# Performance work log

Measured on AMD Instinct MI355X. Metric: run time of the kernel, lower is better.

The kernel has to match this reference:

```python
import jax, jax.numpy as jnp
from jax import lax
import numpy as np


def _conv4d(x, w, b, stride, padding):
    # Faithful 4D conv emulation: K temporal slices, each its own 3D conv.
    # x: [B,Ci,T,D,H,W]; w: [K,Co,Ci,k,k,k]; b: [K,Co] or None.
    # Quirk preserved: bias b[i] is added once per contributing temporal tap i
    # (the torch code accumulates full conv3d outputs including bias).
    B, Ci, T = x.shape[0], x.shape[1], x.shape[2]
    K = w.shape[0]
    O = (T + 2 * padding - K) // stride + 1
    out = None
    for i in range(K):
        j = np.arange(O) * stride + i - padding          # static input frame idx per output frame
        valid = (j >= 0) & (j < T)
        jc = np.clip(j, 0, T - 1)
        xg = jnp.moveaxis(x[:, :, jc], 2, 1)             # [B,O,Ci,D,H,W]
        xg = xg.reshape(B * O, Ci, x.shape[3], x.shape[4], x.shape[5])
        y = lax.conv_general_dilated(xg, w[i], (stride,) * 3, [(padding, padding)] * 3,
                                     dimension_numbers=('NCDHW', 'OIDHW', 'NCDHW'))
        if b is not None:
            y = y + b[i][None, :, None, None, None]
        y = y.reshape(B, O, y.shape[1], y.shape[2], y.shape[3], y.shape[4])
        y = y * jnp.asarray(valid, y.dtype)[None, :, None, None, None, None]
        out = y if out is None else out + y
    return jnp.moveaxis(out, 1, 2)                       # [B,Co,O,D',H',W']


def _maxpool4d(x, k, s, p):
    # pool3d-per-frame then pool1d over T == one 4D max pool (max commutes)
    return lax.reduce_window(x, jnp.array(-jnp.inf, x.dtype), lax.max,
                             (1, 1, k, k, k, k), (1, 1, s, s, s, s),
                             [(0, 0), (0, 0)] + [(p, p)] * 4)


def _avgpool4d_2(x):
    # avg-of-avgs over a full (2,2,2,2) window == 4D average
    s = lax.reduce_window(x, jnp.array(0.0, x.dtype), lax.add,
                          (1, 1, 2, 2, 2, 2), (1,) * 6, [(0, 0)] * 6)
    return s / jnp.asarray(16.0, x.dtype)


def _block(x, w1, b1, w2, b2, stride, dw):
    y = jax.nn.relu(_conv4d(x, w1, b1, stride, 1))
    y = _conv4d(y, w2, b2, 1, 1)
    res = x if dw is None else _conv4d(x, dw, None, stride, 0)
    return jax.nn.relu(y + res)


def _forward(x, conv1_w, l1_w1, l1_b1, l1_w2, l1_b2,
             l2_w1, l2_b1, l2_w2, l2_b2, l2_dw,
             l3_w1, l3_b1, l3_w2, l3_b2, l3_dw,
             l4_w1, l4_b1, l4_w2, l4_b2, l4_dw, fc_w, fc_b):
    h = x[:, None]                                       # [B,1,T,D,H,W]
    h = jax.nn.relu(_conv4d(h, conv1_w, None, 2, 3))     # 36 -> 18
    h = _maxpool4d(h, 3, 2, 1)                           # 18 -> 9
    h = _block(h, l1_w1, l1_b1, l1_w2, l1_b2, 1, None)   # 9
    h = _block(h, l2_w1, l2_b1, l2_w2, l2_b2, 2, l2_dw)  # 9 -> 5
    h = _block(h, l3_w1, l3_b1, l3_w2, l3_b2, 2, l3_dw)  # 5 -> 3
    h = _block(h, l4_w1, l4_b1, l4_w2, l4_b2, 2, l4_dw)  # 3 -> 2
    h = _avgpool4d_2(h)                                  # 2 -> 1
    h = h.reshape(-1, 512)
    return h @ fc_w.T + fc_b


def setup_inputs() -> dict:
    key = jax.random.key(0)
    ks = jax.random.split(key, 40)
    ctr = iter(range(40))
    def w(shape, fan):
        return jax.random.normal(ks[next(ctr)], shape, jnp.float32) * np.float32(np.sqrt(2.0 / fan))
    def bias(shape):
        return jax.random.normal(ks[next(ctr)], shape, jnp.float32) * np.float32(0.01)
    d = {}
    d['x'] = jax.random.normal(ks[next(ctr)], (1, 36, 36, 36, 36), jnp.float32)
    d['conv1_w'] = w((7, 64, 1, 7, 7, 7), 343)
    d['l1_w1'] = w((3, 64, 64, 3, 3, 3), 64 * 27); d['l1_b1'] = bias((3, 64))
    d['l1_w2'] = w((3, 64, 64, 3, 3, 3), 64 * 27); d['l1_b2'] = bias((3, 64))
    d['l2_w1'] = w((3, 128, 64, 3, 3, 3), 64 * 27); d['l2_b1'] = bias((3, 128))
    d['l2_w2'] = w((3, 128, 128, 3, 3, 3), 128 * 27); d['l2_b2'] = bias((3, 128))
    d['l2_dw'] = w((1, 128, 64, 1, 1, 1), 64)
    d['l3_w1'] = w((3, 256, 128, 3, 3, 3), 128 * 27); d['l3_b1'] = bias((3, 256))
    d['l3_w2'] = w((3, 256, 256, 3, 3, 3), 256 * 27); d['l3_b2'] = bias((3, 256))
    d['l3_dw'] = w((1, 256, 128, 1, 1, 1), 128)
    d['l4_w1'] = w((3, 512, 256, 3, 3, 3), 256 * 27); d['l4_b1'] = bias((3, 512))
    d['l4_w2'] = w((3, 512, 512, 3, 3, 3), 512 * 27); d['l4_b2'] = bias((3, 512))
    d['l4_dw'] = w((1, 512, 256, 1, 1, 1), 256)
    d['fc_w'] = w((1, 512), 512); d['fc_b'] = bias((1,))
    return d


def reference(x, conv1_w, l1_w1, l1_b1, l1_w2, l1_b2,
              l2_w1, l2_b1, l2_w2, l2_b2, l2_dw,
              l3_w1, l3_b1, l3_w2, l3_b2, l3_dw,
              l4_w1, l4_b1, l4_w2, l4_b2, l4_dw, fc_w, fc_b):
    return _forward(x, conv1_w, l1_w1, l1_b1, l1_w2, l1_b2,
                    l2_w1, l2_b1, l2_w2, l2_b2, l2_dw,
                    l3_w1, l3_b1, l3_w2, l3_b2, l3_dw,
                    l4_w1, l4_b1, l4_w2, l4_b2, l4_dw, fc_w, fc_b)
```

## Files before the change

kernel.cpp:

```cpp
#include <hip/hip_runtime.h>

typedef __bf16 bf16x8 __attribute__((ext_vector_type(8)));
typedef float f32x4 __attribute__((ext_vector_type(4)));
typedef unsigned short ushortT;

__device__ __forceinline__ unsigned short f2bf(float f) {
    unsigned u = __float_as_uint(f);
    u += 0x7fffu + ((u >> 16) & 1u);
    return (unsigned short)(u >> 16);
}
__device__ __forceinline__ float bf2f(unsigned short h) {
    return __uint_as_float((unsigned)h << 16);
}

__global__ __launch_bounds__(256) void prep0(const float* __restrict__ x,
                                             const float* __restrict__ c1w,
                                             ushortT* __restrict__ xp,
                                             ushortT* __restrict__ o1) {
    int bid = blockIdx.x, tid = threadIdx.x;
    if (bid < 1737) {
        long idx = (long)bid * 256 + tid;
        if (idx >= 444528L) return;
        int q = (int)(idx % 6); long r = idx / 6;
        int h = (int)(r % 42); r /= 42;
        int d = (int)(r % 42); int t = (int)(r / 42);
        int tt = t - 3, dd = d - 3, hh = h - 3;
        bool rok = ((unsigned)tt < 36u) && ((unsigned)dd < 36u) && ((unsigned)hh < 36u);
        const float* src = x + (((long)tt * 36 + dd) * 36 + hh) * 36;
        union { ushortT s[8]; uint4 u; } v;
#pragma unroll
        for (int j = 0; j < 8; ++j) {
            int ww = q * 8 + j - 3;
            float f = (rok && (unsigned)ww < 36u) ? src[ww] : 0.f;
            v.s[j] = f2bf(f);
        }
        *(uint4*)(xp + idx * 8) = v.u;
    } else {
        int e = (bid - 1737) * 256 + tid;
        if (e < 200704) {
            int k = e % 3136, co = e / 3136;
            int kw = k & 7, kh = (k >> 3) & 7, kdt = k >> 6;
            int kt = kdt / 7, kd = kdt % 7;
            float v = 0.f;
            if (kh < 7 && kw < 7)
                v = c1w[(size_t)(kt * 64 + co) * 343 + kd * 49 + kh * 7 + kw];
            o1[e] = f2bf(v);
        }
    }
}

__global__ __launch_bounds__(128) void mega_kernel(
        const ushortT* __restrict__ xp, const ushortT* __restrict__ aw,
        ushortT* __restrict__ outc1,
        const float* __restrict__ w11, const float* __restrict__ w12,
        const float* __restrict__ w21, const float* __restrict__ w22,
        const float* __restrict__ w31, const float* __restrict__ w32,
        const float* __restrict__ w41, const float* __restrict__ w42,
        ushortT* __restrict__ o11, ushortT* __restrict__ o12,
        ushortT* __restrict__ o21, ushortT* __restrict__ o22,
        ushortT* __restrict__ o31, ushortT* __restrict__ o32,
        ushortT* __restrict__ o41, ushortT* __restrict__ o42) {
    __shared__ __align__(16) ushortT smem[10472];
    int bid = blockIdx.x, tid = threadIdx.x;

    if (bid < 1350) {
        int wt = bid % 5; int r = bid / 5;
        int ht = r % 5; r /= 5;
        int dt = r % 3; int ot = r / 3;
        int ow0 = wt * 4, oh0 = ht * 4, od0 = dt * 6;
        int gw0 = 2 * ow0, gh0 = 2 * oh0, gd0 = 2 * od0;

        int lane = tid & 63, wv = tid >> 6;
        int l15 = lane & 15, g = lane >> 4;
        int dh = l15 >> 2, dw = l15 & 3;

        const ushortT* ap0 = aw + (size_t)(wv * 32 + l15) * 3136 + g * 8;
        const ushortT* ap1 = ap0 + 16 * 3136;

        ushortT* curb = smem;
        ushortT* nxtb = smem + 5236;

        auto stage = [&](ushortT* buf, int kt) {
            int gt = 2 * ot + kt;
            for (int rr = tid; rr < 238; rr += 128) {
                int ld = rr / 14, lh = rr - ld * 14;
                const ushortT* s = xp +
                    ((size_t)((gt * 42 + gd0 + ld) * 42 + gh0 + lh)) * 48 + gw0;
                uint4 a = *(const uint4*)s;
                uint4 b = *(const uint4*)(s + 8);
                unsigned* d = (unsigned*)buf + rr * 11;
                d[0] = a.x; d[1] = a.y; d[2] = a.z; d[3] = a.w;
                d[4] = b.x; d[5] = b.y; d[6] = b.z; d[7] = b.w;
            }
        };

        f32x4 acc[2][6];
#pragma unroll
        for (int c = 0; c < 2; ++c)
#pragma unroll
            for (int m = 0; m < 6; ++m) acc[c][m] = (f32x4){0.f, 0.f, 0.f, 0.f};

        stage(curb, 0);
        __syncthreads();

        int lhl = (2 * dh + g) * 22 + 2 * dw;
        int kidx = 0;
        for (int kt = 0; kt < 7; ++kt) {
            if (kt < 6) stage(nxtb, kt + 1);
            for (int kd = 0; kd < 7; ++kd) {
                int C0 = kd * 308 + lhl;
#pragma unroll
                for (int khq = 0; khq < 2; ++khq) {
                    bf16x8 a0 = *(const bf16x8*)(ap0 + kidx);
                    bf16x8 a1 = *(const bf16x8*)(ap1 + kidx);
                    kidx += 32;
                    int C = C0 + khq * 88;
#pragma unroll
                    for (int m = 0; m < 6; ++m) {
                        int off = C + m * 616;
                        union { unsigned u[4]; bf16x8 v; } bb;
                        bb.u[0] = *(const unsigned*)(curb + off);
                        bb.u[1] = *(const unsigned*)(curb + off + 2);
                        bb.u[2] = *(const unsigned*)(curb + off + 4);
                        bb.u[3] = *(const unsigned*)(curb + off + 6);
                        acc[0][m] = __builtin_amdgcn_mfma_f32_16x16x32_bf16(a0, bb.v, acc[0][m], 0, 0, 0);
                        acc[1][m] = __builtin_amdgcn_mfma_f32_16x16x32_bf16(a1, bb.v, acc[1][m], 0, 0, 0);
                    }
                }
            }
            __syncthreads();
            ushortT* t2 = curb; curb = nxtb; nxtb = t2;
        }

        int oh = oh0 + dh, ow = ow0 + dw;
        if (oh < 18 && ow < 18) {
#pragma unroll
            for (int m = 0; m < 6; ++m) {
                int od = od0 + m;
                int pos = ((ot * 18 + od) * 18 + oh) * 18 + ow;
#pragma unroll
                for (int c = 0; c < 2; ++c) {
                    ushort4 st;
                    st.x = f2bf(fmaxf(acc[c][m][0], 0.f));
                    st.y = f2bf(fmaxf(acc[c][m][1], 0.f));
                    st.z = f2bf(fmaxf(acc[c][m][2], 0.f));
                    st.w = f2bf(fmaxf(acc[c][m][3], 0.f));
                    *(ushort4*)(outc1 + (size_t)pos * 64 + wv * 32 + c * 16 + g * 4) = st;
                }
            }
        }
        return;
    }

    int wb = bid - 1350;
    const float* in; ushortT* out; int Ci, Co, nc, base;
    if (wb < 1536) {
        if (wb < 384) {
            if (wb < 192) { in = w11; out = o11; Ci = 64; Co = 64; nc = 1; base = 0; }
            else          { in = w12; out = o12; Ci = 64; Co = 64; nc = 1; base = 192; }
        } else if (wb < 768) { in = w21; out = o21; Ci = 64;  Co = 128; nc = 1; base = 384; }
        else                 { in = w22; out = o22; Ci = 128; Co = 128; nc = 2; base = 768; }
    } else if (wb < 6144) {
        if (wb < 3072) { in = w31; out = o31; Ci = 128; Co = 256; nc = 2; base = 1536; }
        else           { in = w32; out = o32; Ci = 256; Co = 256; nc = 4; base = 3072; }
    } else {
        if (wb < 12288) { in = w41; out = o41; Ci = 256; Co = 512; nc = 4; base = 6144; }
        else            { in = w42; out = o42; Ci = 512; Co = 512; nc = 8; base = 12288; }
    }
    int lb = wb - base;
    int c64 = lb % nc;
    int co = (lb / nc) % Co;
    int i = lb / (nc * Co);

    const float* src = in + ((size_t)(i * Co + co) * Ci + 64 * c64) * 27;
    float* tile = (float*)smem;
    for (int e = tid; e < 432; e += 128)
        *(float4*)(tile + 4 * e) = *(const float4*)(src + 4 * e);
    __syncthreads();
    ushortT* dst = out + (size_t)(i * 27) * Co * Ci + (size_t)co * Ci + 64 * c64;
    size_t tapstride = (size_t)Co * Ci;
    for (int e = tid; e < 432; e += 128) {
        int tap = e >> 4, q = e & 15;
        ushort4 v;
        v.x = f2bf(tile[(4 * q + 0) * 27 + tap]);
        v.y = f2bf(tile[(4 * q + 1) * 27 + tap]);
        v.z = f2bf(tile[(4 * q + 2) * 27 + tap]);
        v.w = f2bf(tile[(4 * q + 3) * 27 + tap]);
        *(ushort4*)(dst + (size_t)tap * tapstride + 4 * q) = v;
    }
}

__global__ void maxpool2(const ushortT* __restrict__ in, ushortT* __restrict__ out,
                         ushortT* __restrict__ zb) {
    int idx = blockIdx.x * 256 + threadIdx.x;
    if (idx < 128) zb[idx] = 0;
    if (idx >= 6561 * 16) return;
    int c4 = idx & 15;
    int p = idx >> 4;
    int ow = p % 9; int t = p / 9;
    int oh = t % 9; t /= 9;
    int od = t % 9; int ot = t / 9;
    ushort4 m = {0, 0, 0, 0};
    for (int kt = 0; kt < 3; ++kt) { int it = 2 * ot + kt - 1; if ((unsigned)it >= 18u) continue;
        for (int kd = 0; kd < 3; ++kd) { int id = 2 * od + kd - 1; if ((unsigned)id >= 18u) continue;
            for (int kh = 0; kh < 3; ++kh) { int ih = 2 * oh + kh - 1; if ((unsigned)ih >= 18u) continue;
                int rb = ((it * 18 + id) * 18 + ih) * 18;
                for (int kw = 0; kw < 3; ++kw) { int iw = 2 * ow + kw - 1; if ((unsigned)iw >= 18u) continue;
                    ushort4 v = *(const ushort4*)(in + (size_t)(rb + iw) * 64 + c4 * 4);
                    m.x = v.x > m.x ? v.x : m.x;
                    m.y = v.y > m.y ? v.y : m.y;
                    m.z = v.z > m.z ? v.z : m.z;
                    m.w = v.w > m.w ? v.w : m.w;
                }
            }
        }
    }
    *(ushort4*)(out + (size_t)p * 64 + c4 * 4) = m;
}

template <int KC, int FUSE>
__global__ void convmfma(const ushortT* __restrict__ xb, const ushortT* __restrict__ wt,
                         const float* __restrict__ bias, const ushortT* __restrict__ res,
                         ushortT* __restrict__ outb, float* __restrict__ part,
                         const ushortT* __restrict__ zq,
                         int Ci, int Co, int T, int O, int stride, int chunk,
                         const float* __restrict__ dwW, ushortT* __restrict__ dwOut) {
    if (dwW && blockIdx.y == (unsigned)(Co >> 6)) {
        int O2 = O * O, O3 = O2 * O, O4 = O3 * O;
        int total = Co * O4;
        int sthr = gridDim.x * gridDim.z * 256;
        for (int idx = (blockIdx.z * gridDim.x + blockIdx.x) * 256 + threadIdx.x;
             idx < total; idx += sthr) {
            int co = idx % Co;
            int pos = idx / Co;
            int ow = pos % O, oh = (pos / O) % O, od = (pos / O2) % O, ot = pos / O3;
            int ip = (((2 * ot) * T + 2 * od) * T + 2 * oh) * T + 2 * ow;
            const ushortT* xpp = xb + (size_t)ip * Ci;
            const float* wp = dwW + (size_t)co * Ci;
            float acc = 0.f;
            for (int c8 = 0; c8 < Ci; c8 += 8) {
                uint4 xv = *(const uint4*)(xpp + c8);
                float4 w0 = *(const float4*)(wp + c8);
                float4 w1 = *(const float4*)(wp + c8 + 4);
                acc = fmaf(bf2f((unsigned short)(xv.x & 0xffff)), w0.x, acc);
                acc = fmaf(bf2f((unsigned short)(xv.x >> 16)),    w0.y, acc);
                acc = fmaf(bf2f((unsigned short)(xv.y & 0xffff)), w0.z, acc);
                acc = fmaf(bf2f((unsigned short)(xv.y >> 16)),    w0.w, acc);
                acc = fmaf(bf2f((unsigned short)(xv.z & 0xffff)), w1.x, acc);
                acc = fmaf(bf2f((unsigned short)(xv.z >> 16)),    w1.y, acc);
                acc = fmaf(bf2f((unsigned short)(xv.w & 0xffff)), w1.z, acc);
                acc = fmaf(bf2f((unsigned short)(xv.w >> 16)),    w1.w, acc);
            }
            dwOut[idx] = f2bf(acc);
        }
        return;
    }

    int lane = threadIdx.x & 63;
    int wv = threadIdx.x >> 6;
    int p0 = blockIdx.x * 16;
    int co0 = (blockIdx.y * 4 + wv) * 16;
    int cbase = blockIdx.z * chunk;

    int pn = p0 + (lane & 15);
    int O2 = O * O, O3 = O2 * O, O4 = O3 * O;
    bool pv = pn < O4;
    int pc = pv ? pn : 0;
    int ow = pc % O, oh = (pc / O) % O, od = (pc / O2) % O, ot = pc / O3;
    int g = lane >> 4;
    int kl = cbase + g * 8;

    const ushortT* aRow = wt + (size_t)(co0 + (lane & 15)) * Ci + kl;
    size_t tapStride = (size_t)Co * Ci;
    const ushortT* zp = zq + g * 8;

    f32x4 acc[4];
#pragma unroll
    for (int a = 0; a < 4; ++a) acc[a] = (f32x4){0.f, 0.f, 0.f, 0.f};

    int itb = ot * stride - 1, idb = od * stride - 1, ihb = oh * stride - 1, iwb = ow * stride - 1;

#pragma unroll
    for (int i = 0; i < 3; ++i) {
        int it = itb + i;
        bool vt = pv && ((unsigned)it < (unsigned)T);
#pragma unroll
        for (int kd = 0; kd < 3; ++kd) {
            int id = idb + kd;
            bool vdd = vt && ((unsigned)id < (unsigned)T);
            int btd = (it * T + id) * T;
#pragma unroll
            for (int kh = 0; kh < 3; ++kh) {
                int ih = ihb + kh;
                bool vh = vdd && ((unsigned)ih < (unsigned)T);
#pragma unroll
                for (int kw = 0; kw < 3; ++kw) {
                    int iw = iwb + kw;
                    bool v = vh && ((unsigned)iw < (unsigned)T);
                    int ip = (btd + ih) * T + iw;
                    const ushortT* bp = v ? (xb + (size_t)ip * Ci + kl) : zp;
                    const int tap = (i * 9 + kd * 3 + kh) * 3 + kw;
                    const ushortT* apw = aRow + (size_t)tap * tapStride;
#pragma unroll
                    for (int kc = 0; kc < KC; ++kc) {
                        bf16x8 av = *(const bf16x8*)(apw + kc * 32);
                        bf16x8 bv = *(const bf16x8*)(bp + kc * 32);
                        acc[(tap * KC + kc) & 3] =
                            __builtin_amdgcn_mfma_f32_16x16x32_bf16(av, bv, acc[(tap * KC + kc) & 3], 0, 0, 0);
                    }
                }
            }
        }
    }

    if (!pv) return;
    f32x4 asum = acc[0];
#pragma unroll
    for (int a = 1; a < 4; ++a) {
        asum[0] += acc[a][0]; asum[1] += acc[a][1];
        asum[2] += acc[a][2]; asum[3] += acc[a][3];
    }
    int cob = co0 + g * 4;
    if (FUSE) {
        float bb[4] = {0.f, 0.f, 0.f, 0.f};
        for (int i = 0; i < 3; ++i) {
            int it = itb + i;
            if ((unsigned)it < (unsigned)T) {
#pragma unroll
                for (int rr = 0; rr < 4; ++rr) bb[rr] += bias[i * Co + cob + rr];
            }
        }
        float rv[4] = {0.f, 0.f, 0.f, 0.f};
        if (res) {
            ushort4 r4 = *(const ushort4*)(res + (size_t)pn * Co + cob);
            rv[0] = bf2f(r4.x); rv[1] = bf2f(r4.y); rv[2] = bf2f(r4.z); rv[3] = bf2f(r4.w);
        }
        ushort4 st;
        st.x = f2bf(fmaxf(asum[0] + bb[0] + rv[0], 0.f));
        st.y = f2bf(fmaxf(asum[1] + bb[1] + rv[1], 0.f));
        st.z = f2bf(fmaxf(asum[2] + bb[2] + rv[2], 0.f));
        st.w = f2bf(fmaxf(asum[3] + bb[3] + rv[3], 0.f));
        *(ushort4*)(outb + (size_t)pn * Co + cob) = st;
    } else {
        *(f32x4*)(part + ((size_t)blockIdx.z * O4 + pn) * Co + cob) = asum;
    }
}

__global__ void finalize_k(const float* __restrict__ part, int KS,
                           const float* __restrict__ bias, const ushortT* __restrict__ res,
                           ushortT* __restrict__ outb, int Co, int O4, int T, int O, int stride,
                           int total) {
    int idx = blockIdx.x * 256 + threadIdx.x;
    if (idx >= total) return;
    int co = idx % Co;
    int pos = idx / Co;
    float v = 0.f;
    for (int z = 0; z < KS; ++z) v += part[((size_t)z * O4 + pos) * Co + co];
    int ot = pos / (O * O * O);
    for (int i = 0; i < 3; ++i) {
        int it = ot * stride + i - 1;
        if ((unsigned)it < (unsigned)T) v += bias[i * Co + co];
    }
    if (res) v += bf2f(res[idx]);
    outb[idx] = f2bf(fmaxf(v, 0.f));
}

__global__ void avgfc2(const ushortT* __restrict__ xin, const float* __restrict__ fw,
                       const float* __restrict__ fb, float* __restrict__ out) {
    __shared__ float ls[8];
    int t = threadIdx.x;
    float s = 0.f;
#pragma unroll
    for (int pp = 0; pp < 16; ++pp) s += bf2f(xin[pp * 512 + t]);
    s = s * (1.f / 16.f) * fw[t];
    for (int off = 32; off > 0; off >>= 1) s += __shfl_xor(s, off, 64);
    if ((t & 63) == 0) ls[t >> 6] = s;
    __syncthreads();
    if (t == 0) {
        float tot = 0.f;
#pragma unroll
        for (int i = 0; i < 8; ++i) tot += ls[i];
        out[0] = tot + fb[0];
    }
}

extern "C" void kernel_launch(void* const* d_in, const int* in_sizes, int n_in,
                              void* d_out, int out_size, void* d_ws, size_t ws_size,
                              hipStream_t stream) {
    const float* x       = (const float*)d_in[0];
    const float* conv1_w = (const float*)d_in[1];
    const float* l1_w1 = (const float*)d_in[2];
    const float* l1_b1 = (const float*)d_in[3];
    const float* l1_w2 = (const float*)d_in[4];
    const float* l1_b2 = (const float*)d_in[5];
    const float* l2_w1 = (const float*)d_in[6];
    const float* l2_b1 = (const float*)d_in[7];
    const float* l2_w2 = (const float*)d_in[8];
    const float* l2_b2 = (const float*)d_in[9];
    const float* l2_dw = (const float*)d_in[10];
    const float* l3_w1 = (const float*)d_in[11];
    const float* l3_b1 = (const float*)d_in[12];
    const float* l3_w2 = (const float*)d_in[13];
    const float* l3_b2 = (const float*)d_in[14];
    const float* l3_dw = (const float*)d_in[15];
    const float* l4_w1 = (const float*)d_in[16];
    const float* l4_b1 = (const float*)d_in[17];
    const float* l4_w2 = (const float*)d_in[18];
    const float* l4_b2 = (const float*)d_in[19];
    const float* l4_dw = (const float*)d_in[20];
    const float* fc_w  = (const float*)d_in[21];
    const float* fc_b  = (const float*)d_in[22];
    float* outp = (float*)d_out;

    char* bp = (char*)d_ws;
    auto alloc = [&](size_t bytes) {
        char* r = bp;
        bp += (bytes + 255) & ~(size_t)255;
        return (void*)r;
    };
    ushortT* A16 = (ushortT*)alloc(6718464ull * 2);
    ushortT* XP  = (ushortT*)alloc(3556224ull * 2);
    ushortT* Aw1 = (ushortT*)alloc(200704ull * 2);
    ushortT* X0 = (ushortT*)alloc(419904ull * 2);
    ushortT* Y1 = (ushortT*)alloc(419904ull * 2);
    ushortT* X1 = (ushortT*)alloc(419904ull * 2);
    ushortT* Y2 = (ushortT*)alloc(80000ull * 2);
    ushortT* R2 = (ushortT*)alloc(80000ull * 2);
    ushortT* X2 = (ushortT*)alloc(80000ull * 2);
    ushortT* Y3 = (ushortT*)alloc(20736ull * 2);
    ushortT* R3 = (ushortT*)alloc(20736ull * 2);
    ushortT* X3 = (ushortT*)alloc(20736ull * 2);
    ushortT* Y4 = (ushortT*)alloc(8192ull * 2);
    ushortT* R4 = (ushortT*)alloc(8192ull * 2);
    ushortT* X4 = (ushortT*)alloc(8192ull * 2);
    ushortT* W11 = (ushortT*)alloc(331776ull * 2);
    ushortT* W12 = (ushortT*)alloc(331776ull * 2);
    ushortT* W21 = (ushortT*)alloc(663552ull * 2);
    ushortT* W22 = (ushortT*)alloc(1327104ull * 2);
    ushortT* W31 = (ushortT*)alloc(2654208ull * 2);
    ushortT* W32 = (ushortT*)alloc(5308416ull * 2);
    ushortT* W41 = (ushortT*)alloc(10616832ull * 2);
    ushortT* W42 = (ushortT*)alloc(21233664ull * 2);
    float* P    = (float*)alloc(165888ull * 4);
    ushortT* ZB = (ushortT*)alloc(256);
    if ((size_t)(bp - (char*)d_ws) > ws_size) return;

    prep0<<<2521, 256, 0, stream>>>(x, conv1_w, XP, Aw1);

    mega_kernel<<<25926, 128, 0, stream>>>(XP, Aw1, A16,
                                           l1_w1, l1_w2, l2_w1, l2_w2, l3_w1, l3_w2,
                                           l4_w1, l4_w2,
                                           W11, W12, W21, W22, W31, W32, W41, W42);

    maxpool2<<<411, 256, 0, stream>>>(A16, X0, ZB);

    convmfma<2, 1><<<dim3(411, 1, 1), 256, 0, stream>>>(X0, W11, l1_b1, nullptr, Y1, nullptr,
                                                        ZB, 64, 64, 9, 9, 1, 64,
                                                        nullptr, nullptr);
    convmfma<2, 1><<<dim3(411, 1, 1), 256, 0, stream>>>(Y1, W12, l1_b2, X0, X1, nullptr,
                                                        ZB, 64, 64, 9, 9, 1, 64,
                                                        nullptr, nullptr);

    convmfma<2, 1><<<dim3(40, 3, 1), 256, 0, stream>>>(X1, W21, l2_b1, nullptr, Y2, nullptr,
                                                       ZB, 64, 128, 9, 5, 2, 64,
                                                       l2_dw, R2);
    convmfma<4, 1><<<dim3(40, 2, 1), 256, 0, stream>>>(Y2, W22, l2_b2, R2, X2, nullptr,
                                                       ZB, 128, 128, 5, 5, 1, 128,
                                                       nullptr, nullptr);

    convmfma<1, 0><<<dim3(6, 5, 4), 256, 0, stream>>>(X2, W31, nullptr, nullptr, nullptr, P,
                                                      ZB, 128, 256, 5, 3, 2, 32,
                                                      l3_dw, R3);
    finalize_k<<<81, 256, 0, stream>>>(P, 4, l3_b1, nullptr, Y3, 256, 81, 5, 3, 2, 20736);
    convmfma<1, 0><<<dim3(6, 4, 8), 256, 0, stream>>>(Y3, W32, nullptr, nullptr, nullptr, P,
                                                      ZB, 256, 256, 3, 3, 1, 32,
                                                      nullptr, nullptr);
    finalize_k<<<81, 256, 0, stream>>>(P, 8, l3_b2, R3, X3, 256, 81, 3, 3, 1, 20736);

    convmfma<1, 0><<<dim3(1, 9, 8), 256, 0, stream>>>(X3, W41, nullptr, nullptr, nullptr, P,
                                                      ZB, 256, 512, 3, 2, 2, 32,
                                                      l4_dw, R4);
    finalize_k<<<32, 256, 0, stream>>>(P, 8, l4_b1, nullptr, Y4, 512, 16, 3, 2, 2, 8192);
    convmfma<1, 0><<<dim3(1, 8, 16), 256, 0, stream>>>(Y4, W42, nullptr, nullptr, nullptr, P,
                                                       ZB, 512, 512, 2, 2, 1, 32,
                                                       nullptr, nullptr);
    finalize_k<<<32, 256, 0, stream>>>(P, 16, l4_b2, R4, X4, 512, 16, 2, 2, 1, 8192);

    avgfc2<<<1, 512, 0, stream>>>(X4, fc_w, fc_b, outp);
}
```

Before: 558.3 us.

## Fuse split-K finalize into consumer convs and precompute per-frame bias sums

The separate finalize kernels for layers 3 and 4 are removed. Each consumer conv (and the final avg+fc kernel) now reduces the split-K partials, adds the precomputed temporal bias sum and residual, and applies ReLU while loading its input operand. Per-output-frame bias sums are computed once in prep0. The mega_kernel shared-memory row pitch also shrinks from 11 to 9 words, cutting LDS footprint. This saves four launches and intermediate bf16 round trips, but the partial sums are recomputed redundantly for every tap that reads them.

```diff
diff --git a/kernel.cpp b/kernel.cpp
--- a/kernel.cpp
+++ b/kernel.cpp
@@ -15,8 +15,16 @@
 
 __global__ __launch_bounds__(256) void prep0(const float* __restrict__ x,
                                              const float* __restrict__ c1w,
+                                             const float* __restrict__ b31,
+                                             const float* __restrict__ b32,
+                                             const float* __restrict__ b41,
+                                             const float* __restrict__ b42,
                                              ushortT* __restrict__ xp,
-                                             ushortT* __restrict__ o1) {
+                                             ushortT* __restrict__ o1,
+                                             float* __restrict__ BS3a,
+                                             float* __restrict__ BS3b,
+                                             float* __restrict__ BS4a,
+                                             float* __restrict__ BS4b) {
     int bid = blockIdx.x, tid = threadIdx.x;
     if (bid < 1737) {
         long idx = (long)bid * 256 + tid;
@@ -35,7 +43,7 @@
             v.s[j] = f2bf(f);
         }
         *(uint4*)(xp + idx * 8) = v.u;
-    } else {
+    } else if (bid < 2521) {
         int e = (bid - 1737) * 256 + tid;
         if (e < 200704) {
             int k = e % 3136, co = e / 3136;
@@ -45,6 +53,29 @@
             if (kh < 7 && kw < 7)
                 v = c1w[(size_t)(kt * 64 + co) * 343 + kd * 49 + kh * 7 + kw];
             o1[e] = f2bf(v);
+        }
+    } else {
+        int e = (bid - 2521) * 256 + tid;
+        if (e >= 3584) return;
+        auto bsum = [&](const float* b, int Co, int ot, int co, int stride, int Tsrc) {
+            float s = 0.f;
+            for (int i = 0; i < 3; ++i) {
+                int it = ot * stride + i - 1;
+                if ((unsigned)it < (unsigned)Tsrc) s += b[i * Co + co];
+            }
+            return s;
+        };
+        if (e < 768) {
+            BS3a[e] = bsum(b31, 256, e / 256, e % 256, 2, 5);
+        } else if (e < 1536) {
+            int e2 = e - 768;
+            BS3b[e2] = bsum(b32, 256, e2 / 256, e2 % 256, 1, 3);
+        } else if (e < 2560) {
+            int e2 = e - 1536;
+            BS4a[e2] = bsum(b41, 512, e2 / 512, e2 % 512, 2, 3);
+        } else {
+            int e2 = e - 2560;
+            BS4b[e2] = bsum(b42, 512, e2 / 512, e2 % 512, 1, 2);
         }
     }
 }
@@ -60,7 +91,7 @@
         ushortT* __restrict__ o21, ushortT* __restrict__ o22,
         ushortT* __restrict__ o31, ushortT* __restrict__ o32,
         ushortT* __restrict__ o41, ushortT* __restrict__ o42) {
-    __shared__ __align__(16) ushortT smem[10472];
+    __shared__ __align__(16) ushortT smem[8568];
     int bid = blockIdx.x, tid = threadIdx.x;
 
     if (bid < 1350) {
@@ -78,7 +109,7 @@
         const ushortT* ap1 = ap0 + 16 * 3136;
 
         ushortT* curb = smem;
-        ushortT* nxtb = smem + 5236;
+        ushortT* nxtb = smem + 4284;
 
         auto stage = [&](ushortT* buf, int kt) {
             int gt = 2 * ot + kt;
@@ -88,7 +119,7 @@
                     ((size_t)((gt * 42 + gd0 + ld) * 42 + gh0 + lh)) * 48 + gw0;
                 uint4 a = *(const uint4*)s;
                 uint4 b = *(const uint4*)(s + 8);
-                unsigned* d = (unsigned*)buf + rr * 11;
+                unsigned* d = (unsigned*)buf + rr * 9;
                 d[0] = a.x; d[1] = a.y; d[2] = a.z; d[3] = a.w;
                 d[4] = b.x; d[5] = b.y; d[6] = b.z; d[7] = b.w;
             }
@@ -103,21 +134,21 @@
         stage(curb, 0);
         __syncthreads();
 
-        int lhl = (2 * dh + g) * 22 + 2 * dw;
+        int lhl = (2 * dh + g) * 18 + 2 * dw;
         int kidx = 0;
         for (int kt = 0; kt < 7; ++kt) {
             if (kt < 6) stage(nxtb, kt + 1);
             for (int kd = 0; kd < 7; ++kd) {
-                int C0 = kd * 308 + lhl;
+                int C0 = kd * 252 + lhl;
 #pragma unroll
                 for (int khq = 0; khq < 2; ++khq) {
                     bf16x8 a0 = *(const bf16x8*)(ap0 + kidx);
                     bf16x8 a1 = *(const bf16x8*)(ap1 + kidx);
                     kidx += 32;
-                    int C = C0 + khq * 88;
+                    int C = C0 + khq * 72;
 #pragma unroll
                     for (int m = 0; m < 6; ++m) {
-                        int off = C + m * 616;
+                        int off = C + m * 504;
                         union { unsigned u[4]; bf16x8 v; } bb;
                         bb.u[0] = *(const unsigned*)(curb + off);
                         bb.u[1] = *(const unsigned*)(curb + off + 2);
@@ -218,13 +249,40 @@
     *(ushort4*)(out + (size_t)p * 64 + c4 * 4) = m;
 }
 
-template <int KC, int FUSE>
+template <int KS>
+__device__ __forceinline__ void fin8f(const float* __restrict__ Pin, int O4p, int Ci,
+                                      int ip, int kl, const float* __restrict__ BS,
+                                      int ot, const ushortT* __restrict__ resf,
+                                      float* s) {
+    const float* bs = BS + ot * Ci + kl;
+#pragma unroll
+    for (int j = 0; j < 8; ++j) s[j] = bs[j];
+    if (resf) {
+#pragma unroll
+        for (int j = 0; j < 8; ++j) s[j] += bf2f(resf[(size_t)ip * Ci + kl + j]);
+    }
+#pragma unroll
+    for (int z = 0; z < KS; ++z) {
+        const float* p = Pin + ((size_t)z * O4p + ip) * Ci + kl;
+        float4 a = *(const float4*)p;
+        float4 b = *(const float4*)(p + 4);
+        s[0] += a.x; s[1] += a.y; s[2] += a.z; s[3] += a.w;
+        s[4] += b.x; s[5] += b.y; s[6] += b.z; s[7] += b.w;
+    }
+#pragma unroll
+    for (int j = 0; j < 8; ++j) s[j] = fmaxf(s[j], 0.f);
+}
+
+template <int KC, int FUSE, int FINKS>
 __global__ void convmfma(const ushortT* __restrict__ xb, const ushortT* __restrict__ wt,
                          const float* __restrict__ bias, const ushortT* __restrict__ res,
                          ushortT* __restrict__ outb, float* __restrict__ part,
                          const ushortT* __restrict__ zq,
                          int Ci, int Co, int T, int O, int stride, int chunk,
-                         const float* __restrict__ dwW, ushortT* __restrict__ dwOut) {
+                         const float* __restrict__ dwW, ushortT* __restrict__ dwOut,
+                         const float* __restrict__ Pin, const float* __restrict__ BS,
+                         const ushortT* __restrict__ resf) {
+    int T2 = T * T, T3 = T2 * T, T4 = T3 * T;
     if (dwW && blockIdx.y == (unsigned)(Co >> 6)) {
         int O2 = O * O, O3 = O2 * O, O4 = O3 * O;
         int total = Co * O4;
@@ -235,21 +293,31 @@
             int pos = idx / Co;
             int ow = pos % O, oh = (pos / O) % O, od = (pos / O2) % O, ot = pos / O3;
             int ip = (((2 * ot) * T + 2 * od) * T + 2 * oh) * T + 2 * ow;
-            const ushortT* xpp = xb + (size_t)ip * Ci;
             const float* wp = dwW + (size_t)co * Ci;
             float acc = 0.f;
-            for (int c8 = 0; c8 < Ci; c8 += 8) {
-                uint4 xv = *(const uint4*)(xpp + c8);
-                float4 w0 = *(const float4*)(wp + c8);
-                float4 w1 = *(const float4*)(wp + c8 + 4);
-                acc = fmaf(bf2f((unsigned short)(xv.x & 0xffff)), w0.x, acc);
-                acc = fmaf(bf2f((unsigned short)(xv.x >> 16)),    w0.y, acc);
-                acc = fmaf(bf2f((unsigned short)(xv.y & 0xffff)), w0.z, acc);
-                acc = fmaf(bf2f((unsigned short)(xv.y >> 16)),    w0.w, acc);
-                acc = fmaf(bf2f((unsigned short)(xv.z & 0xffff)), w1.x, acc);
-                acc = fmaf(bf2f((unsigned short)(xv.z >> 16)),    w1.y, acc);
-                acc = fmaf(bf2f((unsigned short)(xv.w & 0xffff)), w1.z, acc);
-                acc = fmaf(bf2f((unsigned short)(xv.w >> 16)),    w1.w, acc);
+            if constexpr (FINKS == 0) {
+                const ushortT* xpp = xb + (size_t)ip * Ci;
+                for (int c8 = 0; c8 < Ci; c8 += 8) {
+                    uint4 xv = *(const uint4*)(xpp + c8);
+                    float4 w0 = *(const float4*)(wp + c8);
+                    float4 w1 = *(const float4*)(wp + c8 + 4);
+                    acc = fmaf(bf2f((unsigned short)(xv.x & 0xffff)), w0.x, acc);
+                    acc = fmaf(bf2f((unsigned short)(xv.x >> 16)),    w0.y, acc);
+                    acc = fmaf(bf2f((unsigned short)(xv.y & 0xffff)), w0.z, acc);
+                    acc = fmaf(bf2f((unsigned short)(xv.y >> 16)),    w0.w, acc);
+                    acc = fmaf(bf2f((unsigned short)(xv.z & 0xffff)), w1.x, acc);
+                    acc = fmaf(bf2f((unsigned short)(xv.z >> 16)),    w1.y, acc);
+                    acc = fmaf(bf2f((unsigned short)(xv.w & 0xffff)), w1.z, acc);
+                    acc = fmaf(bf2f((unsigned short)(xv.w >> 16)),    w1.w, acc);
+                }
+            } else {
+                int ots = ip / T3;
+                for (int c8 = 0; c8 < Ci; c8 += 8) {
+                    float s[8];
+                    fin8f<FINKS>(Pin, T4, Ci, ip, c8, BS, ots, resf, s);
+#pragma unroll
+                    for (int j = 0; j < 8; ++j) acc = fmaf(s[j], wp[c8 + j], acc);
+                }
             }
             dwOut[idx] = f2bf(acc);
         }
@@ -298,13 +366,25 @@
                     int iw = iwb + kw;
                     bool v = vh && ((unsigned)iw < (unsigned)T);
                     int ip = (btd + ih) * T + iw;
-                    const ushortT* bp = v ? (xb + (size_t)ip * Ci + kl) : zp;
                     const int tap = (i * 9 + kd * 3 + kh) * 3 + kw;
                     const ushortT* apw = aRow + (size_t)tap * tapStride;
 #pragma unroll
                     for (int kc = 0; kc < KC; ++kc) {
                         bf16x8 av = *(const bf16x8*)(apw + kc * 32);
-                        bf16x8 bv = *(const bf16x8*)(bp + kc * 32);
+                        bf16x8 bv;
+                        if constexpr (FINKS == 0) {
+                            const ushortT* bp = v ? (xb + (size_t)ip * Ci + kl) : zp;
+                            bv = *(const bf16x8*)(bp + kc * 32);
+                        } else {
+                            int ipc = v ? ip : 0;
+                            float s[8];
+                            fin8f<FINKS>(Pin, T4, Ci, ipc, kl + kc * 32, BS, ipc / T3, resf, s);
+                            union { ushortT u[8]; bf16x8 v8; } rb;
+#pragma unroll
+                            for (int j = 0; j < 8; ++j)
+                                rb.u[j] = v ? f2bf(s[j]) : (ushortT)0;
+                            bv = rb.v8;
+                        }
                         acc[(tap * KC + kc) & 3] =
                             __builtin_amdgcn_mfma_f32_16x16x32_bf16(av, bv, acc[(tap * KC + kc) & 3], 0, 0, 0);
                     }
@@ -314,12 +394,10 @@
     }
 
     if (!pv) return;
-    f32x4 asum = acc[0];
-#pragma unroll
-    for (int a = 1; a < 4; ++a) {
-        asum[0] += acc[a][0]; asum[1] += acc[a][1];
-        asum[2] += acc[a][2]; asum[3] += acc[a][3];
-    }
+    f32x4 asum;
+#pragma unroll
+    for (int r = 0; r < 4; ++r)
+        asum[r] = (acc[0][r] + acc[1][r]) + (acc[2][r] + acc[3][r]);
     int cob = co0 + g * 4;
     if (FUSE) {
         float bb[4] = {0.f, 0.f, 0.f, 0.f};
@@ -346,32 +424,18 @@
     }
 }
 
-__global__ void finalize_k(const float* __restrict__ part, int KS,
-                           const float* __restrict__ bias, const ushortT* __restrict__ res,
-                           ushortT* __restrict__ outb, int Co, int O4, int T, int O, int stride,
-                           int total) {
-    int idx = blockIdx.x * 256 + threadIdx.x;
-    if (idx >= total) return;
-    int co = idx % Co;
-    int pos = idx / Co;
-    float v = 0.f;
-    for (int z = 0; z < KS; ++z) v += part[((size_t)z * O4 + pos) * Co + co];
-    int ot = pos / (O * O * O);
-    for (int i = 0; i < 3; ++i) {
-        int it = ot * stride + i - 1;
-        if ((unsigned)it < (unsigned)T) v += bias[i * Co + co];
-    }
-    if (res) v += bf2f(res[idx]);
-    outb[idx] = f2bf(fmaxf(v, 0.f));
-}
-
-__global__ void avgfc2(const ushortT* __restrict__ xin, const float* __restrict__ fw,
-                       const float* __restrict__ fb, float* __restrict__ out) {
+__global__ void avgfc3(const float* __restrict__ Pin, const float* __restrict__ BS,
+                       const ushortT* __restrict__ R4,
+                       const float* __restrict__ fw, const float* __restrict__ fb,
+                       float* __restrict__ out) {
     __shared__ float ls[8];
     int t = threadIdx.x;
     float s = 0.f;
-#pragma unroll
-    for (int pp = 0; pp < 16; ++pp) s += bf2f(xin[pp * 512 + t]);
+    for (int pp = 0; pp < 16; ++pp) {
+        float v = BS[(pp >> 3) * 512 + t] + bf2f(R4[pp * 512 + t]);
+        for (int z = 0; z < 16; ++z) v += Pin[((size_t)z * 16 + pp) * 512 + t];
+        s += fmaxf(v, 0.f);
+    }
     s = s * (1.f / 16.f) * fw[t];
     for (int off = 32; off > 0; off >>= 1) s += __shfl_xor(s, off, 64);
     if ((t & 63) == 0) ls[t >> 6] = s;
@@ -427,12 +491,8 @@
     ushortT* Y2 = (ushortT*)alloc(80000ull * 2);
     ushortT* R2 = (ushortT*)alloc(80000ull * 2);
     ushortT* X2 = (ushortT*)alloc(80000ull * 2);
-    ushortT* Y3 = (ushortT*)alloc(20736ull * 2);
     ushortT* R3 = (ushortT*)alloc(20736ull * 2);
-    ushortT* X3 = (ushortT*)alloc(20736ull * 2);
-    ushortT* Y4 = (ushortT*)alloc(8192ull * 2);
     ushortT* R4 = (ushortT*)alloc(8192ull * 2);
-    ushortT* X4 = (ushortT*)alloc(8192ull * 2);
     ushortT* W11 = (ushortT*)alloc(331776ull * 2);
     ushortT* W12 = (ushortT*)alloc(331776ull * 2);
     ushortT* W21 = (ushortT*)alloc(663552ull * 2);
@@ -441,11 +501,17 @@
     ushortT* W32 = (ushortT*)alloc(5308416ull * 2);
     ushortT* W41 = (ushortT*)alloc(10616832ull * 2);
     ushortT* W42 = (ushortT*)alloc(21233664ull * 2);
-    float* P    = (float*)alloc(165888ull * 4);
+    float* PA   = (float*)alloc(82944ull * 4);
+    float* PB   = (float*)alloc(165888ull * 4);
+    float* BS3a = (float*)alloc(768ull * 4);
+    float* BS3b = (float*)alloc(768ull * 4);
+    float* BS4a = (float*)alloc(1024ull * 4);
+    float* BS4b = (float*)alloc(1024ull * 4);
     ushortT* ZB = (ushortT*)alloc(256);
     if ((size_t)(bp - (char*)d_ws) > ws_size) return;
 
-    prep0<<<2521, 256, 0, stream>>>(x, conv1_w, XP, Aw1);
+    prep0<<<2535, 256, 0, stream>>>(x, conv1_w, l3_b1, l3_b2, l4_b1, l4_b2,
+                                    XP, Aw1, BS3a, BS3b, BS4a, BS4b);
 
     mega_kernel<<<25926, 128, 0, stream>>>(XP, Aw1, A16,
                                            l1_w1, l1_w2, l2_w1, l2_w2, l3_w1, l3_w2,
@@ -454,37 +520,33 @@
 
     maxpool2<<<411, 256, 0, stream>>>(A16, X0, ZB);
 
-    convmfma<2, 1><<<dim3(411, 1, 1), 256, 0, stream>>>(X0, W11, l1_b1, nullptr, Y1, nullptr,
-                                                        ZB, 64, 64, 9, 9, 1, 64,
-                                                        nullptr, nullptr);
-    convmfma<2, 1><<<dim3(411, 1, 1), 256, 0, stream>>>(Y1, W12, l1_b2, X0, X1, nullptr,
-                                                        ZB, 64, 64, 9, 9, 1, 64,
-                                                        nullptr, nullptr);
-
-    convmfma<2, 1><<<dim3(40, 3, 1), 256, 0, stream>>>(X1, W21, l2_b1, nullptr, Y2, nullptr,
-                                                       ZB, 64, 128, 9, 5, 2, 64,
-                                                       l2_dw, R2);
-    convmfma<4, 1><<<dim3(40, 2, 1), 256, 0, stream>>>(Y2, W22, l2_b2, R2, X2, nullptr,
-                                                       ZB, 128, 128, 5, 5, 1, 128,
-                                                       nullptr, nullptr);
-
-    convmfma<1, 0><<<dim3(6, 5, 4), 256, 0, stream>>>(X2, W31, nullptr, nullptr, nullptr, P,
-                                                      ZB, 128, 256, 5, 3, 2, 32,
-                                                      l3_dw, R3);
-    finalize_k<<<81, 256, 0, stream>>>(P, 4, l3_b1, nullptr, Y3, 256, 81, 5, 3, 2, 20736);
-    convmfma<1, 0><<<dim3(6, 4, 8), 256, 0, stream>>>(Y3, W32, nullptr, nullptr, nullptr, P,
-                                                      ZB, 256, 256, 3, 3, 1, 32,
-                                                      nullptr, nullptr);
-    finalize_k<<<81, 256, 0, stream>>>(P, 8, l3_b2, R3, X3, 256, 81, 3, 3, 1, 20736);
-
-    convmfma<1, 0><<<dim3(1, 9, 8), 256, 0, stream>>>(X3, W41, nullptr, nullptr, nullptr, P,
-                                                      ZB, 256, 512, 3, 2, 2, 32,
-                                                      l4_dw, R4);
-    finalize_k<<<32, 256, 0, stream>>>(P, 8, l4_b1, nullptr, Y4, 512, 16, 3, 2, 2, 8192);
-    convmfma<1, 0><<<dim3(1, 8, 16), 256, 0, stream>>>(Y4, W42, nullptr, nullptr, nullptr, P,
-                                                       ZB, 512, 512, 2, 2, 1, 32,
-                                                       nullptr, nullptr);
-    finalize_k<<<32, 256, 0, stream>>>(P, 16, l4_b2, R4, X4, 512, 16, 2, 2, 1, 8192);
-
-    avgfc2<<<1, 512, 0, stream>>>(X4, fc_w, fc_b, outp);
-}
+    convmfma<2, 1, 0><<<dim3(411, 1, 1), 256, 0, stream>>>(
+        X0, W11, l1_b1, nullptr, Y1, nullptr, ZB, 64, 64, 9, 9, 1, 64,
+        nullptr, nullptr, nullptr, nullptr, nullptr);
+    convmfma<2, 1, 0><<<dim3(411, 1, 1), 256, 0, stream>>>(
+        Y1, W12, l1_b2, X0, X1, nullptr, ZB, 64, 64, 9, 9, 1, 64,
+        nullptr, nullptr, nullptr, nullptr, nullptr);
+
+    convmfma<2, 1, 0><<<dim3(40, 3, 1), 256, 0, stream>>>(
+        X1, W21, l2_b1, nullptr, Y2, nullptr, ZB, 64, 128, 9, 5, 2, 64,
+        l2_dw, R2, nullptr, nullptr, nullptr);
+    convmfma<4, 1, 0><<<dim3(40, 2, 1), 256, 0, stream>>>(
+        Y2, W22, l2_b2, R2, X2, nullptr, ZB, 128, 128, 5, 5, 1, 128,
+        nullptr, nullptr, nullptr, nullptr, nullptr);
+
+    convmfma<1, 0, 0><<<dim3(6, 5, 4), 256, 0, stream>>>(
+        X2, W31, nullptr, nullptr, nullptr, PA, ZB, 128, 256, 5, 3, 2, 32,
+        l3_dw, R3, nullptr, nullptr, nullptr);
+    convmfma<1, 0, 4><<<dim3(6, 4, 8), 256, 0, stream>>>(
+        nullptr, W32, nullptr, nullptr, nullptr, PB, ZB, 256, 256, 3, 3, 1, 32,
+        nullptr, nullptr, PA, BS3a, nullptr);
+
+    convmfma<1, 0, 8><<<dim3(1, 9, 8), 256, 0, stream>>>(
+        nullptr, W41, nullptr, nullptr, nullptr, PA, ZB, 256, 512, 3, 2, 2, 32,
+        l4_dw, R4, PB, BS3b, R3);
+    convmfma<1, 0, 8><<<dim3(1, 8, 16), 256, 0, stream>>>(
+        nullptr, W42, nullptr, nullptr, nullptr, PB, ZB, 512, 512, 2, 2, 1, 32,
+        nullptr, nullptr, PA, BS4a, nullptr);
+
+    avgfc3<<<1, 512, 0, stream>>>(PB, BS4b, R4, fc_w, fc_b, outp);
+}
```

Measured after the change: 798.8 us. 1.43x slower.

## Pre-tile weights into MFMA fragment layout and split layer3/4 convs over taps

Applied to the files above, without the earlier changes.

The weight conversion now writes bf16 weights already arranged as 16x32 MFMA A-fragments, so each lane loads a contiguous 16-byte chunk instead of strided rows. Layer 3 and 4 convolutions are additionally split across 9 (time, depth) tap groups through a new TS template parameter, which multiplies grid size and the number of partial sums the finalize kernel reduces. The stem kernel's LDS row padding drops from 11 to 9 words, reducing shared memory per block. The trade-offs are a much larger partial buffer and more finalize reduction traffic, plus a possible change in LDS bank conflicts.

```diff
diff --git a/kernel.cpp b/kernel.cpp
--- a/kernel.cpp
+++ b/kernel.cpp
@@ -60,7 +60,7 @@
         ushortT* __restrict__ o21, ushortT* __restrict__ o22,
         ushortT* __restrict__ o31, ushortT* __restrict__ o32,
         ushortT* __restrict__ o41, ushortT* __restrict__ o42) {
-    __shared__ __align__(16) ushortT smem[10472];
+    __shared__ __align__(16) ushortT smem[8568];
     int bid = blockIdx.x, tid = threadIdx.x;
 
     if (bid < 1350) {
@@ -78,7 +78,7 @@
         const ushortT* ap1 = ap0 + 16 * 3136;
 
         ushortT* curb = smem;
-        ushortT* nxtb = smem + 5236;
+        ushortT* nxtb = smem + 4284;
 
         auto stage = [&](ushortT* buf, int kt) {
             int gt = 2 * ot + kt;
@@ -88,7 +88,7 @@
                     ((size_t)((gt * 42 + gd0 + ld) * 42 + gh0 + lh)) * 48 + gw0;
                 uint4 a = *(const uint4*)s;
                 uint4 b = *(const uint4*)(s + 8);
-                unsigned* d = (unsigned*)buf + rr * 11;
+                unsigned* d = (unsigned*)buf + rr * 9;
                 d[0] = a.x; d[1] = a.y; d[2] = a.z; d[3] = a.w;
                 d[4] = b.x; d[5] = b.y; d[6] = b.z; d[7] = b.w;
             }
@@ -103,21 +103,21 @@
         stage(curb, 0);
         __syncthreads();
 
-        int lhl = (2 * dh + g) * 22 + 2 * dw;
+        int lhl = (2 * dh + g) * 18 + 2 * dw;
         int kidx = 0;
         for (int kt = 0; kt < 7; ++kt) {
             if (kt < 6) stage(nxtb, kt + 1);
             for (int kd = 0; kd < 7; ++kd) {
-                int C0 = kd * 308 + lhl;
+                int C0 = kd * 252 + lhl;
 #pragma unroll
                 for (int khq = 0; khq < 2; ++khq) {
                     bf16x8 a0 = *(const bf16x8*)(ap0 + kidx);
                     bf16x8 a1 = *(const bf16x8*)(ap1 + kidx);
                     kidx += 32;
-                    int C = C0 + khq * 88;
+                    int C = C0 + khq * 72;
 #pragma unroll
                     for (int m = 0; m < 6; ++m) {
-                        int off = C + m * 616;
+                        int off = C + m * 504;
                         union { unsigned u[4]; bf16x8 v; } bb;
                         bb.u[0] = *(const unsigned*)(curb + off);
                         bb.u[1] = *(const unsigned*)(curb + off + 2);
@@ -177,16 +177,19 @@
     for (int e = tid; e < 432; e += 128)
         *(float4*)(tile + 4 * e) = *(const float4*)(src + 4 * e);
     __syncthreads();
-    ushortT* dst = out + (size_t)(i * 27) * Co * Ci + (size_t)co * Ci + 64 * c64;
-    size_t tapstride = (size_t)Co * Ci;
-    for (int e = tid; e < 432; e += 128) {
-        int tap = e >> 4, q = e & 15;
-        ushort4 v;
-        v.x = f2bf(tile[(4 * q + 0) * 27 + tap]);
-        v.y = f2bf(tile[(4 * q + 1) * 27 + tap]);
-        v.z = f2bf(tile[(4 * q + 2) * 27 + tap]);
-        v.w = f2bf(tile[(4 * q + 3) * 27 + tap]);
-        *(ushort4*)(dst + (size_t)tap * tapstride + 4 * q) = v;
+
+    size_t nCb = Co >> 4, nKb = Ci >> 5;
+    int cb = co >> 4, l15 = co & 15;
+    for (int e = tid; e < 216; e += 128) {
+        int tap = e >> 3, q8 = e & 7;
+        int kb = 2 * c64 + (q8 >> 2);
+        int g = q8 & 3;
+        int tapP = i * 27 + tap;
+        union { ushortT s[8]; uint4 u; } v;
+#pragma unroll
+        for (int j = 0; j < 8; ++j)
+            v.s[j] = f2bf(tile[(q8 * 8 + j) * 27 + tap]);
+        *(uint4*)(out + (((size_t)tapP * nCb + cb) * nKb + kb) * 512 + (g * 16 + l15) * 8) = v.u;
     }
 }
 
@@ -218,7 +221,7 @@
     *(ushort4*)(out + (size_t)p * 64 + c4 * 4) = m;
 }
 
-template <int KC, int FUSE>
+template <int KC, int FUSE, int TS>
 __global__ void convmfma(const ushortT* __restrict__ xb, const ushortT* __restrict__ wt,
                          const float* __restrict__ bias, const ushortT* __restrict__ res,
                          ushortT* __restrict__ outb, float* __restrict__ part,
@@ -259,8 +262,14 @@
     int lane = threadIdx.x & 63;
     int wv = threadIdx.x >> 6;
     int p0 = blockIdx.x * 16;
-    int co0 = (blockIdx.y * 4 + wv) * 16;
-    int cbase = blockIdx.z * chunk;
+    int cb = blockIdx.y * 4 + wv;
+    int co0 = cb * 16;
+    int zz = blockIdx.z;
+    int ks, ts;
+    if (TS > 1) { ks = zz / TS; ts = zz % TS; } else { ks = zz; ts = 0; }
+    int cbase = ks * chunk;
+    int kb0 = cbase >> 5;
+    size_t nCb = Co >> 4, nKb = Ci >> 5;
 
     int pn = p0 + (lane & 15);
     int O2 = O * O, O3 = O2 * O, O4 = O3 * O;
@@ -270,8 +279,6 @@
     int g = lane >> 4;
     int kl = cbase + g * 8;
 
-    const ushortT* aRow = wt + (size_t)(co0 + (lane & 15)) * Ci + kl;
-    size_t tapStride = (size_t)Co * Ci;
     const ushortT* zp = zq + g * 8;
 
     f32x4 acc[4];
@@ -280,46 +287,78 @@
 
     int itb = ot * stride - 1, idb = od * stride - 1, ihb = oh * stride - 1, iwb = ow * stride - 1;
 
-#pragma unroll
-    for (int i = 0; i < 3; ++i) {
-        int it = itb + i;
-        bool vt = pv && ((unsigned)it < (unsigned)T);
-#pragma unroll
-        for (int kd = 0; kd < 3; ++kd) {
-            int id = idb + kd;
-            bool vdd = vt && ((unsigned)id < (unsigned)T);
-            int btd = (it * T + id) * T;
-#pragma unroll
-            for (int kh = 0; kh < 3; ++kh) {
-                int ih = ihb + kh;
-                bool vh = vdd && ((unsigned)ih < (unsigned)T);
-#pragma unroll
-                for (int kw = 0; kw < 3; ++kw) {
-                    int iw = iwb + kw;
-                    bool v = vh && ((unsigned)iw < (unsigned)T);
-                    int ip = (btd + ih) * T + iw;
-                    const ushortT* bp = v ? (xb + (size_t)ip * Ci + kl) : zp;
-                    const int tap = (i * 9 + kd * 3 + kh) * 3 + kw;
-                    const ushortT* apw = aRow + (size_t)tap * tapStride;
-#pragma unroll
-                    for (int kc = 0; kc < KC; ++kc) {
-                        bf16x8 av = *(const bf16x8*)(apw + kc * 32);
-                        bf16x8 bv = *(const bf16x8*)(bp + kc * 32);
-                        acc[(tap * KC + kc) & 3] =
-                            __builtin_amdgcn_mfma_f32_16x16x32_bf16(av, bv, acc[(tap * KC + kc) & 3], 0, 0, 0);
+    if (TS == 1) {
+#pragma unroll
+        for (int i = 0; i < 3; ++i) {
+            int it = itb + i;
+            bool vt = pv && ((unsigned)it < (unsigned)T);
+#pragma unroll
+            for (int kd = 0; kd < 3; ++kd) {
+                int id = idb + kd;
+                bool vdd = vt && ((unsigned)id < (unsigned)T);
+                int btd = (it * T + id) * T;
+#pragma unroll
+                for (int kh = 0; kh < 3; ++kh) {
+                    int ih = ihb + kh;
+                    bool vh = vdd && ((unsigned)ih < (unsigned)T);
+#pragma unroll
+                    for (int kw = 0; kw < 3; ++kw) {
+                        int iw = iwb + kw;
+                        bool v = vh && ((unsigned)iw < (unsigned)T);
+                        int ip = (btd + ih) * T + iw;
+                        const int tap = (i * 9 + kd * 3 + kh) * 3 + kw;
+                        const ushortT* bp = v ? (xb + (size_t)ip * Ci + kl) : zp;
+                        const ushortT* ap = wt + (((size_t)tap * nCb + cb) * nKb + kb0) * 512
+                                            + lane * 8;
+#pragma unroll
+                        for (int kc = 0; kc < KC; ++kc) {
+                            bf16x8 av = *(const bf16x8*)(ap + kc * 512);
+                            bf16x8 bv = *(const bf16x8*)(bp + kc * 32);
+                            acc[(tap * KC + kc) & 3] =
+                                __builtin_amdgcn_mfma_f32_16x16x32_bf16(av, bv,
+                                    acc[(tap * KC + kc) & 3], 0, 0, 0);
+                        }
                     }
                 }
             }
         }
+    } else {
+        int i = ts / 3, kd = ts % 3;
+        int it = itb + i;
+        int id = idb + kd;
+        bool vt = pv && ((unsigned)it < (unsigned)T) && ((unsigned)id < (unsigned)T);
+        int btd = (it * T + id) * T;
+        int tapb = i * 27 + kd * 9;
+#pragma unroll
+        for (int kh = 0; kh < 3; ++kh) {
+            int ih = ihb + kh;
+            bool vh = vt && ((unsigned)ih < (unsigned)T);
+#pragma unroll
+            for (int kw = 0; kw < 3; ++kw) {
+                int iw = iwb + kw;
+                bool v = vh && ((unsigned)iw < (unsigned)T);
+                int ip = (btd + ih) * T + iw;
+                int tap = tapb + kh * 3 + kw;
+                const ushortT* bp = v ? (xb + (size_t)ip * Ci + kl) : zp;
+                const ushortT* ap = wt + (((size_t)tap * nCb + cb) * nKb + kb0) * 512
+                                    + lane * 8;
+#pragma unroll
+                for (int kc = 0; kc < KC; ++kc) {
+                    bf16x8 av = *(const bf16x8*)(ap + kc * 512);
+                    bf16x8 bv = *(const bf16x8*)(bp + kc * 32);
+                    acc[(kh * 3 + kw + kc) & 3] =
+                        __builtin_amdgcn_mfma_f32_16x16x32_bf16(av, bv,
+                            acc[(kh * 3 + kw + kc) & 3], 0, 0, 0);
+                }
+            }
+        }
     }
 
     if (!pv) return;
-    f32x4 asum = acc[0];
-#pragma unroll
-    for (int a = 1; a < 4; ++a) {
-        asum[0] += acc[a][0]; asum[1] += acc[a][1];
-        asum[2] += acc[a][2]; asum[3] += acc[a][3];
-    }
+    f32x4 asum;
+#pragma unroll
+    for (int r = 0; r < 4; ++r)
+        asum[r] = (acc[0][r] + acc[1][r]) + (acc[2][r] + acc[3][r]);
     int cob = co0 + g * 4;
     if (FUSE) {
         float bb[4] = {0.f, 0.f, 0.f, 0.f};
@@ -342,7 +381,7 @@
         st.w = f2bf(fmaxf(asum[3] + bb[3] + rv[3], 0.f));
         *(ushort4*)(outb + (size_t)pn * Co + cob) = st;
     } else {
-        *(f32x4*)(part + ((size_t)blockIdx.z * O4 + pn) * Co + cob) = asum;
+        *(f32x4*)(part + ((size_t)zz * O4 + pn) * Co + cob) = asum;
     }
 }
 
@@ -441,7 +480,7 @@
     ushortT* W32 = (ushortT*)alloc(5308416ull * 2);
     ushortT* W41 = (ushortT*)alloc(10616832ull * 2);
     ushortT* W42 = (ushortT*)alloc(21233664ull * 2);
-    float* P    = (float*)alloc(165888ull * 4);
+    float* P    = (float*)alloc(1492992ull * 4);
     ushortT* ZB = (ushortT*)alloc(256);
     if ((size_t)(bp - (char*)d_ws) > ws_size) return;
 
@@ -454,37 +493,29 @@
 
     maxpool2<<<411, 256, 0, stream>>>(A16, X0, ZB);
 
-    convmfma<2, 1><<<dim3(411, 1, 1), 256, 0, stream>>>(X0, W11, l1_b1, nullptr, Y1, nullptr,
-                                                        ZB, 64, 64, 9, 9, 1, 64,
-                                                        nullptr, nullptr);
-    convmfma<2, 1><<<dim3(411, 1, 1), 256, 0, stream>>>(Y1, W12, l1_b2, X0, X1, nullptr,
-                                                        ZB, 64, 64, 9, 9, 1, 64,
-                                                        nullptr, nullptr);
-
-    convmfma<2, 1><<<dim3(40, 3, 1), 256, 0, stream>>>(X1, W21, l2_b1, nullptr, Y2, nullptr,
-                                                       ZB, 64, 128, 9, 5, 2, 64,
-                                                       l2_dw, R2);
-    convmfma<4, 1><<<dim3(40, 2, 1), 256, 0, stream>>>(Y2, W22, l2_b2, R2, X2, nullptr,
-                                                       ZB, 128, 128, 5, 5, 1, 128,
-                                                       nullptr, nullptr);
-
-    convmfma<1, 0><<<dim3(6, 5, 4), 256, 0, stream>>>(X2, W31, nullptr, nullptr, nullptr, P,
-                                                      ZB, 128, 256, 5, 3, 2, 32,
-                                                      l3_dw, R3);
-    finalize_k<<<81, 256, 0, stream>>>(P, 4, l3_b1, nullptr, Y3, 256, 81, 5, 3, 2, 20736);
-    convmfma<1, 0><<<dim3(6, 4, 8), 256, 0, stream>>>(Y3, W32, nullptr, nullptr, nullptr, P,
-                                                      ZB, 256, 256, 3, 3, 1, 32,
-                                                      nullptr, nullptr);
-    finalize_k<<<81, 256, 0, stream>>>(P, 8, l3_b2, R3, X3, 256, 81, 3, 3, 1, 20736);
-
-    convmfma<1, 0><<<dim3(1, 9, 8), 256, 0, stream>>>(X3, W41, nullptr, nullptr, nullptr, P,
-                                                      ZB, 256, 512, 3, 2, 2, 32,
-                                                      l4_dw, R4);
-    finalize_k<<<32, 256, 0, stream>>>(P, 8, l4_b1, nullptr, Y4, 512, 16, 3, 2, 2, 8192);
-    convmfma<1, 0><<<dim3(1, 8, 16), 256, 0, stream>>>(Y4, W42, nullptr, nullptr, nullptr, P,
-                                                       ZB, 512, 512, 2, 2, 1, 32,
-                                                       nullptr, nullptr);
-    finalize_k<<<32, 256, 0, stream>>>(P, 16, l4_b2, R4, X4, 512, 16, 2, 2, 1, 8192);
+    convmfma<2, 1, 1><<<dim3(411, 1, 1), 256, 0, stream>>>(
+        X0, W11, l1_b1, nullptr, Y1, nullptr, ZB, 64, 64, 9, 9, 1, 64, nullptr, nullptr);
+    convmfma<2, 1, 1><<<dim3(411, 1, 1), 256, 0, stream>>>(
+        Y1, W12, l1_b2, X0, X1, nullptr, ZB, 64, 64, 9, 9, 1, 64, nullptr, nullptr);
+
+    convmfma<2, 1, 1><<<dim3(40, 3, 1), 256, 0, stream>>>(
+        X1, W21, l2_b1, nullptr, Y2, nullptr, ZB, 64, 128, 9, 5, 2, 64, l2_dw, R2);
+    convmfma<4, 1, 1><<<dim3(40, 2, 1), 256, 0, stream>>>(
+        Y2, W22, l2_b2, R2, X2, nullptr, ZB, 128, 128, 5, 5, 1, 128, nullptr, nullptr);
+
+    convmfma<1, 0, 9><<<dim3(6, 5, 36), 256, 0, stream>>>(
+        X2, W31, nullptr, nullptr, nullptr, P, ZB, 128, 256, 5, 3, 2, 32, l3_dw, R3);
+    finalize_k<<<81, 256, 0, stream>>>(P, 36, l3_b1, nullptr, Y3, 256, 81, 5, 3, 2, 20736);
+    convmfma<1, 0, 9><<<dim3(6, 4, 72), 256, 0, stream>>>(
+        Y3, W32, nullptr, nullptr, nullptr, P, ZB, 256, 256, 3, 3, 1, 32, nullptr, nullptr);
+    finalize_k<<<81, 256, 0, stream>>>(P, 72, l3_b2, R3, X3, 256, 81, 3, 3, 1, 20736);
+
+    convmfma<1, 0, 9><<<dim3(1, 9, 72), 256, 0, stream>>>(
+        X3, W41, nullptr, nullptr, nullptr, P, ZB, 256, 512, 3, 2, 2, 32, l4_dw, R4);
+    finalize_k<<<32, 256, 0, stream>>>(P, 72, l4_b1, nullptr, Y4, 512, 16, 3, 2, 2, 8192);
+    convmfma<1, 0, 9><<<dim3(1, 8, 144), 256, 0, stream>>>(
+        Y4, W42, nullptr, nullptr, nullptr, P, ZB, 512, 512, 2, 2, 1, 32, nullptr, nullptr);
+    finalize_k<<<32, 256, 0, stream>>>(P, 144, l4_b2, R4, X4, 512, 16, 2, 2, 1, 8192);
 
     avgfc2<<<1, 512, 0, stream>>>(X4, fc_w, fc_b, outp);
 }
```

Result: faster. 481.0 us (-13.9%).
